# Kernel optimization log

Measured on AMD Instinct MI355X. Metric: run time of the kernel, lower is better.

## Reference

```python
import jax, jax.numpy as jnp
import numpy as np

NUM_FIELDS = 32
EMBED_DIM = 64
BATCH = 4096


def setup_inputs() -> dict:
    key = jax.random.key(0)
    kx, kw = jax.random.split(key)
    x = jax.random.normal(kx, (BATCH, NUM_FIELDS, EMBED_DIM), dtype=jnp.float32)
    # xavier_normal for [input_dim, input_dim]: std = sqrt(2/(fan_in+fan_out))
    std = float(np.sqrt(2.0 / (EMBED_DIM + EMBED_DIM)))
    W = jax.random.normal(kw, (EMBED_DIM, EMBED_DIM), dtype=jnp.float32) * std
    return {"x": x, "W": W}


def reference(x, W):
    # x: [B, F, D], W: [D, D]
    vid = jnp.einsum('bfd,de->bfe', x, W)  # [B, F, D]
    F_ = x.shape[1]
    idx_i, idx_j = jnp.triu_indices(F_, k=1)  # each [P] with P = F*(F-1)/2
    # pairwise Hadamard: x[:, i] * vid[:, j] for all i<j -> [B, P, D]
    return x[:, idx_i, :] * vid[:, idx_j, :]
```

## Files before the change

kernel.cpp:

```cpp
#include <hip/hip_runtime.h>

#define NF 32
#define ED 64
#define NPAIR 496
#define XPAD 68
#define OUT_PER_B (NPAIR * ED)

__global__ __launch_bounds__(256, 4) void bilinear_kernel(
    const float* __restrict__ x, const float* __restrict__ W,
    float* __restrict__ out) {
  __shared__ float xs[NF * XPAD];
  __shared__ float vs[NF * XPAD];
  __shared__ float ws[ED * ED];
  __shared__ int   ptab[NPAIR];

  const int t = threadIdx.x;
  const int b = blockIdx.x;

  for (int p = t; p < NPAIR; p += 256) {
    int i = 0, rem = p;
    while (rem >= (NF - 1 - i)) { rem -= (NF - 1 - i); ++i; }
    ptab[p] = (i << 8) | (i + 1 + rem);
  }

  {
    const float4* Wg = (const float4*)W;
#pragma unroll
    for (int k = 0; k < 4; ++k) {
      int c = t + k * 256;
      float4 v = Wg[c];
      *(float4*)&ws[c * 4] = v;
    }
  }

  {
    const float4* xg = (const float4*)(x + (size_t)b * (NF * ED));
#pragma unroll
    for (int k = 0; k < 2; ++k) {
      int c = t + k * 256;
      int f = c >> 4, d4 = c & 15;
      float4 v = xg[c];
      *(float4*)&xs[f * XPAD + d4 * 4] = v;
    }
  }
  __syncthreads();

  {
    const int f0 = (t >> 4) * 2;
    const int e0 = (t & 15) * 4;
    float4 acc0 = {0.f, 0.f, 0.f, 0.f};
    float4 acc1 = {0.f, 0.f, 0.f, 0.f};
    const float* xr0 = &xs[f0 * XPAD];
    const float* xr1 = &xs[(f0 + 1) * XPAD];
#pragma unroll 8
    for (int d = 0; d < ED; ++d) {
      float a0 = xr0[d];
      float a1 = xr1[d];
      float4 w4 = *(const float4*)&ws[d * ED + e0];
      acc0.x += a0 * w4.x; acc0.y += a0 * w4.y;
      acc0.z += a0 * w4.z; acc0.w += a0 * w4.w;
      acc1.x += a1 * w4.x; acc1.y += a1 * w4.y;
      acc1.z += a1 * w4.z; acc1.w += a1 * w4.w;
    }
    *(float4*)&vs[f0 * XPAD + e0] = acc0;
    *(float4*)&vs[(f0 + 1) * XPAD + e0] = acc1;
  }
  __syncthreads();

  float* ob = out + (size_t)b * OUT_PER_B;
#pragma unroll 4
  for (int it = 0; it < OUT_PER_B / (256 * 4); ++it) {
    int f4 = it * 256 + t;
    int p = f4 >> 4;
    int e = (f4 & 15) * 4;
    int pr = ptab[p];
    int i = pr >> 8, j = pr & 255;
    float4 xv = *(const float4*)&xs[i * XPAD + e];
    float4 vv = *(const float4*)&vs[j * XPAD + e];
    float4 r;
    r.x = xv.x * vv.x; r.y = xv.y * vv.y;
    r.z = xv.z * vv.z; r.w = xv.w * vv.w;
    *(float4*)&ob[(size_t)f4 * 4] = r;
  }
}

extern "C" void kernel_launch(void* const* d_in, const int* in_sizes, int n_in,
                              void* d_out, int out_size, void* d_ws, size_t ws_size,
                              hipStream_t stream) {
  const float* x = (const float*)d_in[0];
  const float* W = (const float*)d_in[1];
  float* out = (float*)d_out;
  const int B = in_sizes[0] / (NF * ED);
  bilinear_kernel<<<B, 256, 0, stream>>>(x, W, out);
}
```

Measured before the change: 600.8 us.

## Split vid GEMM and pairwise expansion into separate kernels with nontemporal stores

Splits the fused kernel into two. The first computes vid = x·W per batch and writes it to global workspace, or into the tail of each batch's output slab if no workspace is available. The second kernel loads x and vid into shared memory and writes the pairwise products with nontemporal stores. It drops the W staging from the store-bound phase and uses a higher occupancy hint, to lighten the expand kernel and stream the large output better. In exchange it adds an extra global round trip for vid and a second launch, and it removes the shared-memory row padding, which may cause bank conflicts in the GEMM.

```diff
diff --git a/kernel.cpp b/kernel.cpp
--- a/kernel.cpp
+++ b/kernel.cpp
@@ -3,17 +3,64 @@
 #define NF 32
 #define ED 64
 #define NPAIR 496
-#define XPAD 68
+#define VID_PER_B (NF * ED)
 #define OUT_PER_B (NPAIR * ED)
 
-__global__ __launch_bounds__(256, 4) void bilinear_kernel(
+typedef float f32x4 __attribute__((ext_vector_type(4)));
+
+__global__ __launch_bounds__(256, 4) void vid_gemm_kernel(
     const float* __restrict__ x, const float* __restrict__ W,
+    float* __restrict__ vid, size_t vstride) {
+  __shared__ float xs[NF * ED];
+  __shared__ float ws[ED * ED];
+  const int t = threadIdx.x;
+  const int b = blockIdx.x;
+
+  {
+    const float4* Wg = (const float4*)W;
+#pragma unroll
+    for (int k = 0; k < 4; ++k) {
+      int c = t + k * 256;
+      *(float4*)&ws[c * 4] = Wg[c];
+    }
+  }
+  {
+    const float4* xg = (const float4*)(x + (size_t)b * VID_PER_B);
+#pragma unroll
+    for (int k = 0; k < 2; ++k) {
+      int c = t + k * 256;
+      *(float4*)&xs[c * 4] = xg[c];
+    }
+  }
+  __syncthreads();
+
+  const int f0 = (t >> 4) * 2;
+  const int e0 = (t & 15) * 4;
+  float4 acc0 = {0.f, 0.f, 0.f, 0.f};
+  float4 acc1 = {0.f, 0.f, 0.f, 0.f};
+  const float* xr0 = &xs[f0 * ED];
+  const float* xr1 = &xs[(f0 + 1) * ED];
+#pragma unroll 8
+  for (int d = 0; d < ED; ++d) {
+    float a0 = xr0[d];
+    float a1 = xr1[d];
+    float4 w4 = *(const float4*)&ws[d * ED + e0];
+    acc0.x += a0 * w4.x; acc0.y += a0 * w4.y;
+    acc0.z += a0 * w4.z; acc0.w += a0 * w4.w;
+    acc1.x += a1 * w4.x; acc1.y += a1 * w4.y;
+    acc1.z += a1 * w4.z; acc1.w += a1 * w4.w;
+  }
+  float* vb = vid + (size_t)b * vstride;
+  *(float4*)&vb[f0 * ED + e0] = acc0;
+  *(float4*)&vb[(f0 + 1) * ED + e0] = acc1;
+}
+
+__global__ __launch_bounds__(256, 8) void expand_kernel(
+    const float* __restrict__ x, const float* __restrict__ vid, size_t vstride,
     float* __restrict__ out) {
-  __shared__ float xs[NF * XPAD];
-  __shared__ float vs[NF * XPAD];
-  __shared__ float ws[ED * ED];
-  __shared__ int   ptab[NPAIR];
-
+  __shared__ float xs[NF * ED];
+  __shared__ float vs[NF * ED];
+  __shared__ int ptab[NPAIR];
   const int t = threadIdx.x;
   const int b = blockIdx.x;
 
@@ -22,65 +69,30 @@
     while (rem >= (NF - 1 - i)) { rem -= (NF - 1 - i); ++i; }
     ptab[p] = (i << 8) | (i + 1 + rem);
   }
-
   {
-    const float4* Wg = (const float4*)W;
-#pragma unroll
-    for (int k = 0; k < 4; ++k) {
-      int c = t + k * 256;
-      float4 v = Wg[c];
-      *(float4*)&ws[c * 4] = v;
-    }
-  }
-
-  {
-    const float4* xg = (const float4*)(x + (size_t)b * (NF * ED));
+    const float4* xg = (const float4*)(x + (size_t)b * VID_PER_B);
+    const float4* vg = (const float4*)(vid + (size_t)b * vstride);
 #pragma unroll
     for (int k = 0; k < 2; ++k) {
       int c = t + k * 256;
-      int f = c >> 4, d4 = c & 15;
-      float4 v = xg[c];
-      *(float4*)&xs[f * XPAD + d4 * 4] = v;
+      *(float4*)&xs[c * 4] = xg[c];
+      *(float4*)&vs[c * 4] = vg[c];
     }
   }
   __syncthreads();
 
-  {
-    const int f0 = (t >> 4) * 2;
-    const int e0 = (t & 15) * 4;
-    float4 acc0 = {0.f, 0.f, 0.f, 0.f};
-    float4 acc1 = {0.f, 0.f, 0.f, 0.f};
-    const float* xr0 = &xs[f0 * XPAD];
-    const float* xr1 = &xs[(f0 + 1) * XPAD];
-#pragma unroll 8
-    for (int d = 0; d < ED; ++d) {
-      float a0 = xr0[d];
-      float a1 = xr1[d];
-      float4 w4 = *(const float4*)&ws[d * ED + e0];
-      acc0.x += a0 * w4.x; acc0.y += a0 * w4.y;
-      acc0.z += a0 * w4.z; acc0.w += a0 * w4.w;
-      acc1.x += a1 * w4.x; acc1.y += a1 * w4.y;
-      acc1.z += a1 * w4.z; acc1.w += a1 * w4.w;
-    }
-    *(float4*)&vs[f0 * XPAD + e0] = acc0;
-    *(float4*)&vs[(f0 + 1) * XPAD + e0] = acc1;
-  }
-  __syncthreads();
-
   float* ob = out + (size_t)b * OUT_PER_B;
+  const int g = t >> 4;
+  const int e = (t & 15) * 4;
 #pragma unroll 4
-  for (int it = 0; it < OUT_PER_B / (256 * 4); ++it) {
-    int f4 = it * 256 + t;
-    int p = f4 >> 4;
-    int e = (f4 & 15) * 4;
+  for (int it = 0; it < NPAIR / 16; ++it) {
+    int p = it * 16 + g;
     int pr = ptab[p];
     int i = pr >> 8, j = pr & 255;
-    float4 xv = *(const float4*)&xs[i * XPAD + e];
-    float4 vv = *(const float4*)&vs[j * XPAD + e];
-    float4 r;
-    r.x = xv.x * vv.x; r.y = xv.y * vv.y;
-    r.z = xv.z * vv.z; r.w = xv.w * vv.w;
-    *(float4*)&ob[(size_t)f4 * 4] = r;
+    f32x4 xv = *(const f32x4*)&xs[i * ED + e];
+    f32x4 vv = *(const f32x4*)&vs[j * ED + e];
+    f32x4 r = xv * vv;
+    __builtin_nontemporal_store(r, (f32x4*)&ob[(size_t)p * ED + e]);
   }
 }
 
@@ -91,5 +103,18 @@
   const float* W = (const float*)d_in[1];
   float* out = (float*)d_out;
   const int B = in_sizes[0] / (NF * ED);
-  bilinear_kernel<<<B, 256, 0, stream>>>(x, W, out);
+
+  const size_t vid_bytes = (size_t)B * VID_PER_B * sizeof(float);
+  float* vid;
+  size_t vstride;
+  if (d_ws != nullptr && ws_size >= vid_bytes) {
+    vid = (float*)d_ws;
+    vstride = VID_PER_B;
+  } else {
+    vid = out + (OUT_PER_B - VID_PER_B);
+    vstride = OUT_PER_B;
+  }
+
+  vid_gemm_kernel<<<B, 256, 0, stream>>>(x, W, vid, vstride);
+  expand_kernel<<<B, 256, 0, stream>>>(x, vid, vstride, out);
 }
```

Result: faster. 540.5 us (-10.0%).
